# Kernel optimization log

Hardware: AMD Instinct MI355X
Metric: run time of the kernel (lower is better)

The kernel has to match this reference:

```python
import jax, jax.numpy as jnp
import numpy as np

# LinearMoELayer(input_size=2048, output_size=2048, num_experts=8, num_selects=2,
#                bias=True, gate_network='mlp', gate_use_balance=True,
#                gate_add_noise=True, gate_use_softmax=True)
# Eval-mode forward semantics (deterministic: noise branch only active in training).
B, S, D, O, E, K = 4, 2048, 2048, 2048, 8, 2
BAL_W = 1e-2   # balance_loss_weight
EPS = 1e-10    # cv_squared eps


def setup_inputs() -> dict:
    key = jax.random.key(0)
    ks = jax.random.split(key, 5)
    x = jax.random.normal(ks[0], (B, S, D), dtype=jnp.float32)
    # gate 'mlp': Linear(D,E,bias=False) -> tanh -> Linear(E,E,bias=False)
    gate_w1 = jax.random.normal(ks[1], (E, D), dtype=jnp.float32) * (1.0 / np.sqrt(D))
    gate_w2 = jax.random.normal(ks[2], (E, E), dtype=jnp.float32) * (1.0 / np.sqrt(E))
    # LinearExperts: per-expert weight [E, O, D] and bias [E, O] (F.linear convention)
    expert_w = jax.random.normal(ks[3], (E, O, D), dtype=jnp.float32) * (1.0 / np.sqrt(D))
    expert_b = jax.random.normal(ks[4], (E, O), dtype=jnp.float32) * 0.01
    return {"x": x, "gate_w1": gate_w1, "gate_w2": gate_w2,
            "expert_w": expert_w, "expert_b": expert_b}


def _cv_squared(v):
    # torch: v.var() / (v.mean()**2 + eps); torch.var is unbiased (ddof=1)
    m = jnp.mean(v)
    var = jnp.sum((v - m) ** 2) / (v.shape[0] - 1)
    return var / (m * m + EPS)


def reference(x, gate_w1, gate_w2, expert_w, expert_b):
    xt = x.reshape(-1, D)                                  # [T, D]
    T = xt.shape[0]
    # --- TopKBalancedNoisyGate (eval path) ---
    logits = jnp.tanh(xt @ gate_w1.T) @ gate_w2.T          # [T, E]
    top_logits, top_idx = jax.lax.top_k(logits, K)         # [T, K]
    scores = jax.nn.softmax(top_logits.astype(jnp.float32), axis=-1)  # [T, K]
    # scatter top-k scores into dense [T, E] gate matrix
    dense = jnp.zeros((T, E), dtype=scores.dtype)
    dense = dense.at[jnp.arange(T)[:, None], top_idx].set(scores)
    importance = dense.sum(axis=0)                         # [E]
    load = (dense > 0).sum(axis=0).astype(jnp.float32)     # [E] token counts
    gate_loss = BAL_W * (_cv_squared(importance) + _cv_squared(load))
    # --- UniversalCalculator: per-expert linear + score-weighted combine ---
    # math-equivalent to sort/dispatch/grouped-linear/index_add combine
    h = jnp.einsum('td,eod->teo', xt, expert_w) + expert_b[None, :, :]  # [T, E, O]
    y = jnp.einsum('te,teo->to', dense, h)                 # [T, O]
    return y.reshape(B, S, O), gate_loss
```

## Files before the change

kernel.cpp:

```cpp
#include <hip/hip_runtime.h>
#include <hip/hip_bf16.h>

#define TT 8192
#define DD 2048
#define OO 2048
#define EE 8

typedef __attribute__((ext_vector_type(4))) float f32x4;
typedef __attribute__((ext_vector_type(8))) short s16x8;
typedef __attribute__((ext_vector_type(4))) short s16x4;

__device__ __forceinline__ short f2bf(float f) {
    union { float f; unsigned u; } v; v.f = f;
    unsigned r = (v.u + 0x7FFFu + ((v.u >> 16) & 1u)) >> 16;
    return (short)(unsigned short)r;
}
__device__ __forceinline__ float bf2f(short s) {
    union { unsigned u; float f; } v; v.u = ((unsigned)(unsigned short)s) << 16;
    return v.f;
}

__global__ __launch_bounds__(256) void cvt_bf16_kernel(const float* __restrict__ in,
                                                       short* __restrict__ out, long n8) {
    long i = (long)blockIdx.x * blockDim.x + threadIdx.x;
    long stride = (long)gridDim.x * blockDim.x;
    for (; i < n8; i += stride) {
        f32x4 a = ((const f32x4*)in)[i * 2];
        f32x4 b = ((const f32x4*)in)[i * 2 + 1];
        s16x8 r;
        r[0] = f2bf(a[0]); r[1] = f2bf(a[1]); r[2] = f2bf(a[2]); r[3] = f2bf(a[3]);
        r[4] = f2bf(b[0]); r[5] = f2bf(b[1]); r[6] = f2bf(b[2]); r[7] = f2bf(b[3]);
        ((s16x8*)out)[i] = r;
    }
}

__global__ __launch_bounds__(256) void gate_kernel(
    const float* __restrict__ x, const float* __restrict__ w1, const float* __restrict__ w2,
    int* __restrict__ tk_idx, float* __restrict__ tk_score)
{
    const int lane = threadIdx.x & 63;
    const int wid = threadIdx.x >> 6;
    const int t = blockIdx.x * 4 + wid;
    const float* xt = x + (long)t * DD;

    float acc[8] = {0.f,0.f,0.f,0.f,0.f,0.f,0.f,0.f};
#pragma unroll
    for (int i = 0; i < DD / 256; ++i) {
        f32x4 xv = *(const f32x4*)&xt[i * 256 + lane * 4];
#pragma unroll
        for (int e2 = 0; e2 < 8; ++e2) {
            f32x4 wv = *(const f32x4*)&w1[e2 * DD + i * 256 + lane * 4];
            acc[e2] += xv[0]*wv[0] + xv[1]*wv[1] + xv[2]*wv[2] + xv[3]*wv[3];
        }
    }
#pragma unroll
    for (int e2 = 0; e2 < 8; ++e2) {
#pragma unroll
        for (int off = 32; off > 0; off >>= 1)
            acc[e2] += __shfl_xor(acc[e2], off, 64);
    }

    float th[8], lg[8];
#pragma unroll
    for (int e2 = 0; e2 < 8; ++e2) th[e2] = tanhf(acc[e2]);
#pragma unroll
    for (int eo = 0; eo < 8; ++eo) {
        float s = 0.f;
#pragma unroll
        for (int e2 = 0; e2 < 8; ++e2) s += th[e2] * w2[eo * 8 + e2];
        lg[eo] = s;
    }
    int e0 = 0;
#pragma unroll
    for (int q = 1; q < 8; ++q) if (lg[q] > lg[e0]) e0 = q;
    int e1 = (e0 == 0) ? 1 : 0;
#pragma unroll
    for (int q = 0; q < 8; ++q) if (q != e0 && lg[q] > lg[e1]) e1 = q;

    float d = expf(lg[e1] - lg[e0]);
    float s0 = 1.f / (1.f + d);
    float s1 = d / (1.f + d);

    if (lane == 0) {
        tk_idx[t * 2] = e0; tk_idx[t * 2 + 1] = e1;
        tk_score[t * 2] = s0; tk_score[t * 2 + 1] = s1;
    }
}

__global__ __launch_bounds__(256) void build_lists(
    const int* __restrict__ tk_idx, const float* __restrict__ tk_score,
    int* __restrict__ tok_list, float* __restrict__ score_list, int* __restrict__ cnt,
    float* __restrict__ imp)
{
    const int e = blockIdx.x;
    const int lane = threadIdx.x & 63;
    const int wid = threadIdx.x >> 6;
    __shared__ int wsum[4];
    __shared__ float wsumF[4];
    int base = 0;
    float ssum = 0.f;
    for (int t0 = 0; t0 < TT; t0 += 256) {
        int t = t0 + threadIdx.x;
        int i0 = tk_idx[t * 2], i1 = tk_idx[t * 2 + 1];
        bool has = (i0 == e) || (i1 == e);
        int slot = (i0 == e) ? 0 : 1;
        float sc = (i0 == e) ? tk_score[t * 2] : tk_score[t * 2 + 1];
        unsigned long long m = __ballot(has);
        int prefix = __popcll(m & ((1ull << lane) - 1ull));
        if (lane == 0) wsum[wid] = __popcll(m);
        __syncthreads();
        int woff = 0;
#pragma unroll
        for (int w = 0; w < 4; ++w) woff += (w < wid) ? wsum[w] : 0;
        int total = wsum[0] + wsum[1] + wsum[2] + wsum[3];
        if (has) {
            int p = base + woff + prefix;
            tok_list[e * TT + p] = t * 2 + slot;
            score_list[e * TT + p] = sc;
            ssum += sc;
        }
        base += total;
        __syncthreads();
    }
#pragma unroll
    for (int off = 32; off > 0; off >>= 1)
        ssum += __shfl_xor(ssum, off, 64);
    if (lane == 0) wsumF[wid] = ssum;
    __syncthreads();
    if (threadIdx.x == 0) {
        cnt[e] = base;
        imp[e] = wsumF[0] + wsumF[1] + wsumF[2] + wsumF[3];
    }
}

__global__ __launch_bounds__(64) void loss_finalize(const float* __restrict__ imp,
                                                    const int* __restrict__ cnt,
                                                    float* __restrict__ loss_out)
{
    if (threadIdx.x == 0) {
        float im[8], ld[8];
        float mi = 0.f, ml = 0.f;
#pragma unroll
        for (int q = 0; q < 8; ++q) {
            im[q] = imp[q]; ld[q] = (float)cnt[q];
            mi += im[q]; ml += ld[q];
        }
        mi *= 0.125f; ml *= 0.125f;
        float vi = 0.f, vl = 0.f;
#pragma unroll
        for (int q = 0; q < 8; ++q) {
            float a = im[q] - mi; vi += a * a;
            float b = ld[q] - ml; vl += b * b;
        }
        vi /= 7.f; vl /= 7.f;
        loss_out[0] = 0.01f * (vi / (mi * mi + 1e-10f) + vl / (ml * ml + 1e-10f));
    }
}

__global__ __launch_bounds__(256) void combine_kernel(float* __restrict__ y,
                                                      const short* __restrict__ part1) {
    long i = (long)blockIdx.x * blockDim.x + threadIdx.x;
    long stride = (long)gridDim.x * blockDim.x;
    const long n4 = (long)TT * OO / 4;
    for (; i < n4; i += stride) {
        f32x4 v = ((const f32x4*)y)[i];
        s16x4 p = ((const s16x4*)part1)[i];
        v[0] += bf2f(p[0]); v[1] += bf2f(p[1]);
        v[2] += bf2f(p[2]); v[3] += bf2f(p[3]);
        ((f32x4*)y)[i] = v;
    }
}

#define GLD16(gsrc, ldst) \
    __builtin_amdgcn_global_load_lds((const __attribute__((address_space(1))) unsigned int*)(gsrc), \
                                     (__attribute__((address_space(3))) unsigned int*)(ldst), 16, 0, 0)

#define BAR()      __builtin_amdgcn_s_barrier()
#define WAIT_LGKM0() do { asm volatile("s_waitcnt lgkmcnt(0)"); \
                          __builtin_amdgcn_sched_barrier(0); } while (0)

__global__ __launch_bounds__(512, 2) void moe_gemm(
    const short* __restrict__ xbf, const short* __restrict__ wbf,
    const float* __restrict__ eb,
    const int* __restrict__ tok_list, const float* __restrict__ score_list,
    const int* __restrict__ cnt, float* __restrict__ y, short* __restrict__ part1)
{
    const int e = blockIdx.z;
    const int n_e = cnt[e];
    const int row0 = blockIdx.y * 256;
    if (row0 >= n_e) return;
    const int col0 = blockIdx.x * 256;

    __shared__ alignas(16) short lds[2 * 32768];
    __shared__ int   stok[256];
    __shared__ float ssc[256];

    const int tid = threadIdx.x;
    const int lane = tid & 63;
    const int wid = tid >> 6;
    const int wr = wid >> 2, wc = wid & 3;
    const int fr = lane & 15, fq = lane >> 4;
    const char* ldsb = (const char*)lds;

    if (tid < 256) {
        int slot = row0 + tid;
        if (slot >= n_e) slot = n_e - 1;
        stok[tid] = tok_list[e * TT + slot];
        ssc[tid]  = score_list[e * TT + slot];
    }
    __syncthreads();

    const int r_ = tid >> 3;
    const int csw = ((tid & 7) ^ (r_ & 7)) * 8;
    const short* aS[4];
#pragma unroll
    for (int g = 0; g < 4; ++g)
        aS[g] = xbf + (long)(stok[g * 64 + r_] >> 1) * DD + csw;
    const short* bS[4];
#pragma unroll
    for (int g = 0; g < 4; ++g)
        bS[g] = wbf + (long)e * OO * DD + (long)(col0 + g * 64 + r_) * DD + csw;

#define STAGE_A(g, kt) GLD16(aS[g] + (kt) * 64, (char*)lds + ((kt) & 1) * 65536 + ((g) * 512 + tid) * 16)
#define STAGE_B(g, kt) GLD16(bS[g] + (kt) * 64, (char*)lds + ((kt) & 1) * 65536 + 32768 + ((g) * 512 + tid) * 16)

    const int aBase = (wr * 128 + fr) * 128;
    const int bBase = 32768 + (wc * 64 + fr) * 128;
    const int sw0 = (fq ^ (fr & 7)) * 16;
    const int sw1 = ((fq + 4) ^ (fr & 7)) * 16;

    f32x4 acc[8][4];
#pragma unroll
    for (int m = 0; m < 8; ++m)
#pragma unroll
        for (int n = 0; n < 4; ++n) acc[m][n] = f32x4{0.f, 0.f, 0.f, 0.f};

    STAGE_A(0, 0); STAGE_A(1, 0); STAGE_A(2, 0); STAGE_A(3, 0);
    STAGE_B(0, 0); STAGE_B(1, 0); STAGE_B(2, 0); STAGE_B(3, 0);
    STAGE_A(0, 1); STAGE_A(1, 1);
    asm volatile("s_waitcnt vmcnt(2)");
    BAR();

    s16x8 a[4][2], b[2][2][2];

#pragma unroll 1
    for (int j = 0; j < DD / 64; ++j) {
        const int fb = (j & 1) * 65536;
        const bool st1 = (j + 1) < DD / 64;
        const bool st2 = (j + 2) < DD / 64;

#pragma unroll
        for (int mm = 0; mm < 4; ++mm) {
            a[mm][0] = *(const s16x8*)(ldsb + fb + aBase + mm * 2048 + sw0);
            a[mm][1] = *(const s16x8*)(ldsb + fb + aBase + mm * 2048 + sw1);
        }
#pragma unroll
        for (int n = 0; n < 2; ++n) {
            b[0][n][0] = *(const s16x8*)(ldsb + fb + bBase + n * 2048 + sw0);
            b[0][n][1] = *(const s16x8*)(ldsb + fb + bBase + n * 2048 + sw1);
        }
        if (st1) { STAGE_A(2, j + 1); STAGE_A(3, j + 1); }
        BAR();
        WAIT_LGKM0();
        __builtin_amdgcn_s_setprio(1);
#pragma unroll
        for (int mm = 0; mm < 4; ++mm)
#pragma unroll
            for (int n = 0; n < 2; ++n) {
                acc[mm][n] = __builtin_amdgcn_mfma_f32_16x16x32_bf16(a[mm][0], b[0][n][0], acc[mm][n], 0, 0, 0);
                acc[mm][n] = __builtin_amdgcn_mfma_f32_16x16x32_bf16(a[mm][1], b[0][n][1], acc[mm][n], 0, 0, 0);
            }
        __builtin_amdgcn_sched_barrier(0);
        __builtin_amdgcn_s_setprio(0);
        BAR();

#pragma unroll
        for (int n = 0; n < 2; ++n) {
            b[1][n][0] = *(const s16x8*)(ldsb + fb + bBase + (2 + n) * 2048 + sw0);
            b[1][n][1] = *(const s16x8*)(ldsb + fb + bBase + (2 + n) * 2048 + sw1);
        }
        if (st1) { STAGE_B(0, j + 1); STAGE_B(1, j + 1); }
        BAR();
        WAIT_LGKM0();
        __builtin_amdgcn_s_setprio(1);
#pragma unroll
        for (int mm = 0; mm < 4; ++mm)
#pragma unroll
            for (int n = 0; n < 2; ++n) {
                acc[mm][2 + n] = __builtin_amdgcn_mfma_f32_16x16x32_bf16(a[mm][0], b[1][n][0], acc[mm][2 + n], 0, 0, 0);
                acc[mm][2 + n] = __builtin_amdgcn_mfma_f32_16x16x32_bf16(a[mm][1], b[1][n][1], acc[mm][2 + n], 0, 0, 0);
            }
        __builtin_amdgcn_sched_barrier(0);
        __builtin_amdgcn_s_setprio(0);
        BAR();

#pragma unroll
        for (int mm = 0; mm < 4; ++mm) {
            a[mm][0] = *(const s16x8*)(ldsb + fb + aBase + 8192 + mm * 2048 + sw0);
            a[mm][1] = *(const s16x8*)(ldsb + fb + aBase + 8192 + mm * 2048 + sw1);
        }
        if (st1) { STAGE_B(2, j + 1); STAGE_B(3, j + 1); }
        BAR();
        WAIT_LGKM0();
        __builtin_amdgcn_s_setprio(1);
#pragma unroll
        for (int mm = 0; mm < 4; ++mm)
#pragma unroll
            for (int n = 0; n < 2; ++n) {
                acc[4 + mm][n] = __builtin_amdgcn_mfma_f32_16x16x32_bf16(a[mm][0], b[0][n][0], acc[4 + mm][n], 0, 0, 0);
                acc[4 + mm][n] = __builtin_amdgcn_mfma_f32_16x16x32_bf16(a[mm][1], b[0][n][1], acc[4 + mm][n], 0, 0, 0);
            }
        __builtin_amdgcn_sched_barrier(0);
        __builtin_amdgcn_s_setprio(0);
        BAR();

        if (st2) { STAGE_A(0, j + 2); STAGE_A(1, j + 2); }
        BAR();
        __builtin_amdgcn_s_setprio(1);
#pragma unroll
        for (int mm = 0; mm < 4; ++mm)
#pragma unroll
            for (int n = 0; n < 2; ++n) {
                acc[4 + mm][2 + n] = __builtin_amdgcn_mfma_f32_16x16x32_bf16(a[mm][0], b[1][n][0], acc[4 + mm][2 + n], 0, 0, 0);
                acc[4 + mm][2 + n] = __builtin_amdgcn_mfma_f32_16x16x32_bf16(a[mm][1], b[1][n][1], acc[4 + mm][2 + n], 0, 0, 0);
            }
        __builtin_amdgcn_sched_barrier(0);
        __builtin_amdgcn_s_setprio(0);
        if (st2) { asm volatile("s_waitcnt vmcnt(2)"); }
        else     { asm volatile("s_waitcnt vmcnt(0)"); }
        __builtin_amdgcn_sched_barrier(0);
        BAR();
    }

    float bval[4];
#pragma unroll
    for (int n = 0; n < 4; ++n)
        bval[n] = eb[e * OO + col0 + wc * 64 + n * 16 + fr];

#pragma unroll
    for (int m = 0; m < 8; ++m) {
#pragma unroll
        for (int jj = 0; jj < 4; ++jj) {
            int tslot = wr * 128 + m * 16 + fq * 4 + jj;
            if (row0 + tslot < n_e) {
                int packed = stok[tslot];
                int t = packed >> 1;
                float s = ssc[tslot];
                if ((packed & 1) == 0) {
#pragma unroll
                    for (int n = 0; n < 4; ++n) {
                        int o = col0 + wc * 64 + n * 16 + fr;
                        y[(long)t * OO + o] = s * (acc[m][n][jj] + bval[n]);
                    }
                } else {
#pragma unroll
                    for (int n = 0; n < 4; ++n) {
                        int o = col0 + wc * 64 + n * 16 + fr;
                        part1[(long)t * OO + o] = f2bf(s * (acc[m][n][jj] + bval[n]));
                    }
                }
            }
        }
    }
#undef STAGE_A
#undef STAGE_B
}

extern "C" void kernel_launch(void* const* d_in, const int* in_sizes, int n_in,
                              void* d_out, int out_size, void* d_ws, size_t ws_size,
                              hipStream_t stream) {
    const float* x  = (const float*)d_in[0];
    const float* w1 = (const float*)d_in[1];
    const float* w2 = (const float*)d_in[2];
    const float* ew = (const float*)d_in[3];
    const float* eb = (const float*)d_in[4];
    float* y = (float*)d_out;

    char* ws = (char*)d_ws;
    short* xbf = (short*)ws;            ws += (size_t)TT * DD * 2;
    short* wbf = (short*)ws;            ws += (size_t)EE * OO * DD * 2;
    short* part1 = (short*)ws;          ws += (size_t)TT * OO * 2;
    int*   tok_list = (int*)ws;         ws += (size_t)EE * TT * 4;
    float* score_list = (float*)ws;     ws += (size_t)EE * TT * 4;
    int*   tk_idx = (int*)ws;           ws += (size_t)TT * 2 * 4;
    float* tk_score = (float*)ws;       ws += (size_t)TT * 2 * 4;
    int*   cnt = (int*)ws;              ws += 64;
    float* imp = (float*)ws;            ws += 64;

    cvt_bf16_kernel<<<4096, 256, 0, stream>>>(ew, wbf, (long)EE * OO * DD / 8);
    cvt_bf16_kernel<<<2048, 256, 0, stream>>>(x,  xbf, (long)TT * DD / 8);
    gate_kernel<<<TT / 4, 256, 0, stream>>>(x, w1, w2, tk_idx, tk_score);
    build_lists<<<EE, 256, 0, stream>>>(tk_idx, tk_score, tok_list, score_list, cnt, imp);
    loss_finalize<<<1, 64, 0, stream>>>(imp, cnt, y + (size_t)TT * OO);
    moe_gemm<<<dim3(OO / 256, TT / 256, EE), 512, 0, stream>>>(
        xbf, wbf, eb, tok_list, score_list, cnt, y, part1);
    combine_kernel<<<2048, 256, 0, stream>>>(y, part1);
}
```

Before: 340.7 us.

## Simplify MoE GEMM main loop schedule and remap block indices for L2 locality

Replaces the four-phase interleaved LDS-read/MFMA schedule (with per-phase barriers, lgkmcnt waits, sched_barriers and setprio) with a simpler loop. Each iteration reads all B fragments and half of A, issues the next-stage loads, runs 32 MFMAs, then reads the second A half and runs the rest. It also swizzles the (row, col) block index so consecutive blocks cover different row tiles of the same column tile, aiming for better weight reuse in L2. The looser schedule leaves instruction interleaving to the compiler, may raise register pressure by holding all B fragments at once, and drops most intra-iteration barriers.

```diff
diff --git a/kernel.cpp b/kernel.cpp
--- a/kernel.cpp
+++ b/kernel.cpp
@@ -175,9 +175,7 @@
     __builtin_amdgcn_global_load_lds((const __attribute__((address_space(1))) unsigned int*)(gsrc), \
                                      (__attribute__((address_space(3))) unsigned int*)(ldst), 16, 0, 0)
 
-#define BAR()      __builtin_amdgcn_s_barrier()
-#define WAIT_LGKM0() do { asm volatile("s_waitcnt lgkmcnt(0)"); \
-                          __builtin_amdgcn_sched_barrier(0); } while (0)
+#define BAR() __builtin_amdgcn_s_barrier()
 
 __global__ __launch_bounds__(512, 2) void moe_gemm(
     const short* __restrict__ xbf, const short* __restrict__ wbf,
@@ -187,9 +185,11 @@
 {
     const int e = blockIdx.z;
     const int n_e = cnt[e];
-    const int row0 = blockIdx.y * 256;
+    const int rc = blockIdx.y * 8 + blockIdx.x;
+    const int rcs = (rc & 7) * 32 + (rc >> 3);
+    const int row0 = (rcs >> 3) * 256;
     if (row0 >= n_e) return;
-    const int col0 = blockIdx.x * 256;
+    const int col0 = (rcs & 7) * 256;
 
     __shared__ alignas(16) short lds[2 * 32768];
     __shared__ int   stok[256];
@@ -241,94 +241,53 @@
     asm volatile("s_waitcnt vmcnt(2)");
     BAR();
 
-    s16x8 a[4][2], b[2][2][2];
-
 #pragma unroll 1
     for (int j = 0; j < DD / 64; ++j) {
         const int fb = (j & 1) * 65536;
         const bool st1 = (j + 1) < DD / 64;
         const bool st2 = (j + 2) < DD / 64;
 
+        s16x8 a0[4][2], a1[4][2], bb[4][2];
+
 #pragma unroll
         for (int mm = 0; mm < 4; ++mm) {
-            a[mm][0] = *(const s16x8*)(ldsb + fb + aBase + mm * 2048 + sw0);
-            a[mm][1] = *(const s16x8*)(ldsb + fb + aBase + mm * 2048 + sw1);
-        }
-#pragma unroll
-        for (int n = 0; n < 2; ++n) {
-            b[0][n][0] = *(const s16x8*)(ldsb + fb + bBase + n * 2048 + sw0);
-            b[0][n][1] = *(const s16x8*)(ldsb + fb + bBase + n * 2048 + sw1);
-        }
-        if (st1) { STAGE_A(2, j + 1); STAGE_A(3, j + 1); }
+            a0[mm][0] = *(const s16x8*)(ldsb + fb + aBase + mm * 2048 + sw0);
+            a0[mm][1] = *(const s16x8*)(ldsb + fb + aBase + mm * 2048 + sw1);
+        }
+#pragma unroll
+        for (int n = 0; n < 4; ++n) {
+            bb[n][0] = *(const s16x8*)(ldsb + fb + bBase + n * 2048 + sw0);
+            bb[n][1] = *(const s16x8*)(ldsb + fb + bBase + n * 2048 + sw1);
+        }
+        if (st1) {
+            STAGE_A(2, j + 1); STAGE_A(3, j + 1);
+            STAGE_B(0, j + 1); STAGE_B(1, j + 1);
+            STAGE_B(2, j + 1); STAGE_B(3, j + 1);
+        }
+#pragma unroll
+        for (int mm = 0; mm < 4; ++mm)
+#pragma unroll
+            for (int n = 0; n < 4; ++n) {
+                acc[mm][n] = __builtin_amdgcn_mfma_f32_16x16x32_bf16(a0[mm][0], bb[n][0], acc[mm][n], 0, 0, 0);
+                acc[mm][n] = __builtin_amdgcn_mfma_f32_16x16x32_bf16(a0[mm][1], bb[n][1], acc[mm][n], 0, 0, 0);
+            }
+#pragma unroll
+        for (int mm = 0; mm < 4; ++mm) {
+            a1[mm][0] = *(const s16x8*)(ldsb + fb + aBase + 8192 + mm * 2048 + sw0);
+            a1[mm][1] = *(const s16x8*)(ldsb + fb + aBase + 8192 + mm * 2048 + sw1);
+        }
+#pragma unroll
+        for (int mm = 0; mm < 4; ++mm)
+#pragma unroll
+            for (int n = 0; n < 4; ++n) {
+                acc[4 + mm][n] = __builtin_amdgcn_mfma_f32_16x16x32_bf16(a1[mm][0], bb[n][0], acc[4 + mm][n], 0, 0, 0);
+                acc[4 + mm][n] = __builtin_amdgcn_mfma_f32_16x16x32_bf16(a1[mm][1], bb[n][1], acc[4 + mm][n], 0, 0, 0);
+            }
+
         BAR();
-        WAIT_LGKM0();
-        __builtin_amdgcn_s_setprio(1);
-#pragma unroll
-        for (int mm = 0; mm < 4; ++mm)
-#pragma unroll
-            for (int n = 0; n < 2; ++n) {
-                acc[mm][n] = __builtin_amdgcn_mfma_f32_16x16x32_bf16(a[mm][0], b[0][n][0], acc[mm][n], 0, 0, 0);
-                acc[mm][n] = __builtin_amdgcn_mfma_f32_16x16x32_bf16(a[mm][1], b[0][n][1], acc[mm][n], 0, 0, 0);
-            }
-        __builtin_amdgcn_sched_barrier(0);
-        __builtin_amdgcn_s_setprio(0);
-        BAR();
-
-#pragma unroll
-        for (int n = 0; n < 2; ++n) {
-            b[1][n][0] = *(const s16x8*)(ldsb + fb + bBase + (2 + n) * 2048 + sw0);
-            b[1][n][1] = *(const s16x8*)(ldsb + fb + bBase + (2 + n) * 2048 + sw1);
-        }
-        if (st1) { STAGE_B(0, j + 1); STAGE_B(1, j + 1); }
-        BAR();
-        WAIT_LGKM0();
-        __builtin_amdgcn_s_setprio(1);
-#pragma unroll
-        for (int mm = 0; mm < 4; ++mm)
-#pragma unroll
-            for (int n = 0; n < 2; ++n) {
-                acc[mm][2 + n] = __builtin_amdgcn_mfma_f32_16x16x32_bf16(a[mm][0], b[1][n][0], acc[mm][2 + n], 0, 0, 0);
-                acc[mm][2 + n] = __builtin_amdgcn_mfma_f32_16x16x32_bf16(a[mm][1], b[1][n][1], acc[mm][2 + n], 0, 0, 0);
-            }
-        __builtin_amdgcn_sched_barrier(0);
-        __builtin_amdgcn_s_setprio(0);
-        BAR();
-
-#pragma unroll
-        for (int mm = 0; mm < 4; ++mm) {
-            a[mm][0] = *(const s16x8*)(ldsb + fb + aBase + 8192 + mm * 2048 + sw0);
-            a[mm][1] = *(const s16x8*)(ldsb + fb + aBase + 8192 + mm * 2048 + sw1);
-        }
-        if (st1) { STAGE_B(2, j + 1); STAGE_B(3, j + 1); }
-        BAR();
-        WAIT_LGKM0();
-        __builtin_amdgcn_s_setprio(1);
-#pragma unroll
-        for (int mm = 0; mm < 4; ++mm)
-#pragma unroll
-            for (int n = 0; n < 2; ++n) {
-                acc[4 + mm][n] = __builtin_amdgcn_mfma_f32_16x16x32_bf16(a[mm][0], b[0][n][0], acc[4 + mm][n], 0, 0, 0);
-                acc[4 + mm][n] = __builtin_amdgcn_mfma_f32_16x16x32_bf16(a[mm][1], b[0][n][1], acc[4 + mm][n], 0, 0, 0);
-            }
-        __builtin_amdgcn_sched_barrier(0);
-        __builtin_amdgcn_s_setprio(0);
-        BAR();
-
         if (st2) { STAGE_A(0, j + 2); STAGE_A(1, j + 2); }
-        BAR();
-        __builtin_amdgcn_s_setprio(1);
-#pragma unroll
-        for (int mm = 0; mm < 4; ++mm)
-#pragma unroll
-            for (int n = 0; n < 2; ++n) {
-                acc[4 + mm][2 + n] = __builtin_amdgcn_mfma_f32_16x16x32_bf16(a[mm][0], b[1][n][0], acc[4 + mm][2 + n], 0, 0, 0);
-                acc[4 + mm][2 + n] = __builtin_amdgcn_mfma_f32_16x16x32_bf16(a[mm][1], b[1][n][1], acc[4 + mm][2 + n], 0, 0, 0);
-            }
-        __builtin_amdgcn_sched_barrier(0);
-        __builtin_amdgcn_s_setprio(0);
         if (st2) { asm volatile("s_waitcnt vmcnt(2)"); }
         else     { asm volatile("s_waitcnt vmcnt(0)"); }
-        __builtin_amdgcn_sched_barrier(0);
         BAR();
     }
 
@@ -392,7 +351,7 @@
     gate_kernel<<<TT / 4, 256, 0, stream>>>(x, w1, w2, tk_idx, tk_score);
     build_lists<<<EE, 256, 0, stream>>>(tk_idx, tk_score, tok_list, score_list, cnt, imp);
     loss_finalize<<<1, 64, 0, stream>>>(imp, cnt, y + (size_t)TT * OO);
-    moe_gemm<<<dim3(OO / 256, TT / 256, EE), 512, 0, stream>>>(
+    moe_gemm<<<dim3(8, TT / 256, EE), 512, 0, stream>>>(
         xbf, wbf, eb, tok_list, score_list, cnt, y, part1);
     combine_kernel<<<2048, 256, 0, stream>>>(y, part1);
 }
```

New measurement: 608.6 us. 78.6% more time.
